# Kernel tuning notes

Measured on AMD Instinct MI355X. Metric: run time of the kernel, lower is better.

## Reference

```python
import jax, jax.numpy as jnp
import numpy as np

B, S, K = 4, 2048, 8
N_NEURONS, N_BASIS, RANK = 64, 32, 8
D_MODEL, D_HID = 256, 1024


def setup_inputs() -> dict:
    key = jax.random.key(0)
    ks = jax.random.split(key, 10)
    x = jax.random.normal(ks[0], (B, S, D_MODEL), dtype=jnp.float32)
    neuron_idx = jax.random.randint(ks[1], (B, S, K), 0, N_NEURONS)
    w = jax.random.uniform(ks[2], (B, S, K), dtype=jnp.float32)
    neuron_weights = w / jnp.sum(w, axis=-1, keepdims=True)  # softmax-like routing weights
    neuron_recipes = jax.random.normal(ks[3], (N_NEURONS, N_BASIS), dtype=jnp.float32) * 0.5
    sc = 0.1
    basis_A1 = jax.random.normal(ks[4], (N_BASIS, 16, RANK, 8), dtype=jnp.float32) * sc
    basis_A2 = jax.random.normal(ks[5], (N_BASIS, RANK, 16, 8), dtype=jnp.float32) * sc
    basis_B1 = jax.random.normal(ks[6], (N_BASIS, 8, RANK, 32), dtype=jnp.float32) * sc
    basis_B2 = jax.random.normal(ks[7], (N_BASIS, RANK, 8, 32), dtype=jnp.float32) * sc
    w_down_w = jax.random.normal(ks[8], (D_HID, D_MODEL), dtype=jnp.float32) * (1.0 / np.sqrt(D_HID))
    w_down_b = jnp.zeros((D_MODEL,), dtype=jnp.float32)
    return {
        "x": x, "neuron_idx": neuron_idx, "neuron_weights": neuron_weights,
        "neuron_recipes": neuron_recipes,
        "basis_A1": basis_A1, "basis_A2": basis_A2,
        "basis_B1": basis_B1, "basis_B2": basis_B2,
        "w_down_w": w_down_w, "w_down_b": w_down_b,
    }


def reference(x, neuron_idx, neuron_weights, neuron_recipes,
              basis_A1, basis_A2, basis_B1, basis_B2, w_down_w, w_down_b):
    Bt, St, D = x.shape
    # --- routing: gather recipes of selected neurons, softmax, weighted-combine ---
    sel = neuron_recipes[neuron_idx]                       # [B,S,k,n_basis]
    sel = jax.nn.softmax(sel, axis=-1)
    wr = jnp.einsum('bskn,bsk->bsn', sel, neuron_weights)  # [B,S,n_basis]
    # --- build per-token TT cores from basis banks (get_neuron_tt_cores) ---
    cA1 = jnp.einsum('bsn,nirk->bsirk', wr, basis_A1)      # [B,S,16,r,8]
    cA2 = jnp.einsum('bsn,nrjl->bsrjl', wr, basis_A2)      # [B,S,r,16,8]
    cB1 = jnp.einsum('bsn,nirk->bsirk', wr, basis_B1)      # [B,S,8,r,32]
    cB2 = jnp.einsum('bsn,nrjl->bsrjl', wr, basis_B2)      # [B,S,r,8,32]
    # --- TT FFN: 256 -> 64 ---
    x_fold = x.reshape(Bt, St, 16, 16)
    temp = jnp.einsum('bsij,bsirk->bsjrk', x_fold, cA1)
    h = jnp.einsum('bsjrk,bsrjl->bskl', temp, cA2).reshape(Bt, St, 64)
    # --- TT FFN: 64 -> 1024 ---
    h_fold = h.reshape(Bt, St, 8, 8)
    temp = jnp.einsum('bsij,bsirk->bsjrk', h_fold, cB1)
    out = jnp.einsum('bsjrk,bsrjl->bskl', temp, cB2).reshape(Bt, St, D_HID)
    out = jax.nn.gelu(out, approximate=False)              # torch F.gelu default = exact erf
    return out @ w_down_w + w_down_b                       # [B,S,256]
```

## Files before the change

kernel.cpp:

```cpp
#include <hip/hip_runtime.h>
#include <math.h>


typedef unsigned short u16;
typedef __attribute__((ext_vector_type(8))) __bf16 bf16x8;
typedef __attribute__((ext_vector_type(4))) float f32x4;
union ABCast { float4 f; bf16x8 v; };
union BFBits { __bf16 b; u16 u; };
union Pack8 { u16 u[8]; float4 f; };

__device__ __forceinline__ float gelu_exact(float v) {
    return 0.5f * v * (1.0f + erff(v * 0.70710678118654752440f));
}
__device__ __forceinline__ u16 f2bf_bits(float f) { BFBits c; c.b = (__bf16)f; return c.u; }
__device__ __forceinline__ float bfbits2f(u16 u) { BFBits c; c.u = u; return (float)c.b; }

__global__ __launch_bounds__(64) void k_route(
    const int* __restrict__ nidx, const float* __restrict__ nw,
    const float* __restrict__ recipes, float* __restrict__ wr_out,
    u16* __restrict__ wrAh, u16* __restrict__ wrAl)
{
    const int t = blockIdx.x * 64 + threadIdx.x;
    float acc[32];
#pragma unroll
    for (int n = 0; n < 32; n++) acc[n] = 0.f;
#pragma unroll
    for (int k = 0; k < 8; k++) {
        const int   id = nidx[t * 8 + k];
        const float wk = nw[t * 8 + k];
        const float4* row = (const float4*)(recipes + id * 32);
        float v[32];
#pragma unroll
        for (int q = 0; q < 8; q++) {
            float4 f = row[q];
            v[q*4+0] = f.x; v[q*4+1] = f.y; v[q*4+2] = f.z; v[q*4+3] = f.w;
        }
        float m = v[0];
#pragma unroll
        for (int n = 1; n < 32; n++) m = fmaxf(m, v[n]);
        float s = 0.f;
#pragma unroll
        for (int n = 0; n < 32; n++) { float e = expf(v[n] - m); v[n] = e; s += e; }
        const float iv = wk / s;
#pragma unroll
        for (int n = 0; n < 32; n++) acc[n] += v[n] * iv;
    }
    float4* o = (float4*)(wr_out + t * 32);
#pragma unroll
    for (int q = 0; q < 8; q++)
        o[q] = make_float4(acc[q*4+0], acc[q*4+1], acc[q*4+2], acc[q*4+3]);

    const int tg16 = t >> 4, tl = t & 15;
#pragma unroll
    for (int c = 0; c < 4; c++) {
        Pack8 ph, pl;
#pragma unroll
        for (int e = 0; e < 8; e++) {
            const float v = acc[c*8 + e];
            const u16 hb = f2bf_bits(v);
            ph.u[e] = hb;
            pl.u[e] = f2bf_bits(v - bfbits2f(hb));
        }
        const int lane = c * 16 + tl;
        *(float4*)(wrAh + (tg16*64 + lane)*8) = ph.f;
        *(float4*)(wrAl + (tg16*64 + lane)*8) = pl.f;
    }
}

__global__ __launch_bounds__(512) void k_stageA(
    const float* __restrict__ x, const float* __restrict__ wr,
    const float* __restrict__ A1, const float* __restrict__ A2,
    float* __restrict__ h_out)
{
    __shared__ float ca[8 * 1024];
    __shared__ float tl[8 * 1088];
    const int tid = threadIdx.x;
    const int t0  = blockIdx.x * 8;
    {
        const int e2 = tid * 2;
        float2 c[8];
#pragma unroll
        for (int tt = 0; tt < 8; tt++) c[tt] = make_float2(0.f, 0.f);
#pragma unroll 4
        for (int n = 0; n < 32; n++) {
            const float2 a = *(const float2*)(A1 + n * 1024 + e2);
#pragma unroll
            for (int tt = 0; tt < 8; tt++) {
                const float s = wr[(t0 + tt) * 32 + n];
                c[tt].x += s * a.x; c[tt].y += s * a.y;
            }
        }
#pragma unroll
        for (int tt = 0; tt < 8; tt++) *(float2*)(ca + tt * 1024 + e2) = c[tt];
    }
    __syncthreads();
    {
        const int t = tid >> 6, g = tid & 63, j = g >> 2, eh = g & 3;
        float xr[16];
#pragma unroll
        for (int i = 0; i < 16; i++) xr[i] = x[(t0 + t) * 256 + i * 16 + j];
        float tr[16];
#pragma unroll
        for (int q = 0; q < 16; q++) tr[q] = 0.f;
#pragma unroll
        for (int i = 0; i < 16; i++) {
            const float xv = xr[i];
#pragma unroll
            for (int q = 0; q < 4; q++) {
                const float4 cv = *(const float4*)(ca + t * 1024 + i * 64 + eh * 16 + q * 4);
                tr[q*4+0] += xv * cv.x; tr[q*4+1] += xv * cv.y;
                tr[q*4+2] += xv * cv.z; tr[q*4+3] += xv * cv.w;
            }
        }
#pragma unroll
        for (int q = 0; q < 4; q++)
            *(float4*)(tl + t * 1088 + j * 68 + eh * 16 + q * 4) =
                make_float4(tr[q*4+0], tr[q*4+1], tr[q*4+2], tr[q*4+3]);
    }
    __syncthreads();
    {
        const int e2 = tid * 2;
        float2 c[8];
#pragma unroll
        for (int tt = 0; tt < 8; tt++) c[tt] = make_float2(0.f, 0.f);
#pragma unroll 4
        for (int n = 0; n < 32; n++) {
            const float2 a = *(const float2*)(A2 + n * 1024 + e2);
#pragma unroll
            for (int tt = 0; tt < 8; tt++) {
                const float s = wr[(t0 + tt) * 32 + n];
                c[tt].x += s * a.x; c[tt].y += s * a.y;
            }
        }
#pragma unroll
        for (int tt = 0; tt < 8; tt++) *(float2*)(ca + tt * 1024 + e2) = c[tt];
    }
    __syncthreads();
    {
        const int t = tid >> 6, g = tid & 63, k = g >> 3, l = g & 7;
        float acc = 0.f;
#pragma unroll
        for (int j = 0; j < 16; j++) {
#pragma unroll
            for (int r = 0; r < 8; r++) {
                acc += tl[t * 1088 + j * 68 + r * 8 + k] *
                       ca[t * 1024 + r * 128 + j * 8 + l];
            }
        }
        h_out[(t0 + t) * 64 + g] = acc;
    }
}

__global__ __launch_bounds__(256) void k_bsplit(
    const float* __restrict__ B1, const float* __restrict__ B2,
    u16* __restrict__ o1h, u16* __restrict__ o1l,
    u16* __restrict__ o2h, u16* __restrict__ o2l)
{
    const int slot = blockIdx.x * 256 + threadIdx.x;
    const int bank = slot >> 13, r = (slot >> 10) & 7, g = (slot >> 6) & 15, l = slot & 63;
    const int c = l & 15, nb = 8 * (l >> 4);
    const int base = (bank == 0)
        ? ((g >> 1) * 256 + r * 32 + (g & 1) * 16 + c)
        : (r * 256 + (g >> 1) * 32 + (g & 1) * 16 + c);
    const float* S = (bank ? B2 : B1) + base + nb * 2048;
    Pack8 ph, pl;
#pragma unroll
    for (int e = 0; e < 8; e++) {
        const float v = S[e * 2048];
        const u16 hb = f2bf_bits(v);
        ph.u[e] = hb;
        pl.u[e] = f2bf_bits(v - bfbits2f(hb));
    }
    const int d = ((r * 16 + g) * 64 + l) * 8;
    *(float4*)((bank ? o2h : o1h) + d) = ph.f;
    *(float4*)((bank ? o2l : o1l) + d) = pl.f;
}

__global__ __launch_bounds__(256) void k_wsplit(
    const float* __restrict__ W, u16* __restrict__ wfh, u16* __restrict__ wfl)
{
    const int slot = blockIdx.x * 256 + threadIdx.x;
    const int ng = slot >> 11, kc = (slot >> 6) & 31, l = slot & 63;
    const float* S = W + (kc * 32 + 8 * (l >> 4)) * 256 + ng * 16 + (l & 15);
    Pack8 ph, pl;
#pragma unroll
    for (int e = 0; e < 8; e++) {
        const float v = S[e * 256];
        const u16 hb = f2bf_bits(v);
        ph.u[e] = hb;
        pl.u[e] = f2bf_bits(v - bfbits2f(hb));
    }
    const int d = ((ng * 32 + kc) * 64 + l) * 8;
    *(float4*)(wfh + d) = ph.f;
    *(float4*)(wfl + d) = pl.f;
}

__global__ __launch_bounds__(1024, 2) void k_fusedB(
    const float* __restrict__ hin,
    const u16* __restrict__ wrAh, const u16* __restrict__ wrAl,
    const u16* __restrict__ bf1h, const u16* __restrict__ bf1l,
    const u16* __restrict__ bf2h, const u16* __restrict__ bf2l,
    const u16* __restrict__ wfh, const u16* __restrict__ wfl,
    const float* __restrict__ bias, float* __restrict__ y)
{
    __shared__ __align__(16) unsigned char smem[81920];
    float* cb1 = (float*)smem;
    float* cb2 = cb1 + 2 * 16 * 256;
    float* t2  = cb2 + 2 * 16 * 256;
    u16* gAh = (u16*)smem;
    u16* gAl = gAh + 16384;

    const int tid = threadIdx.x;
    const int l   = tid & 63;
    const int w   = tid >> 6;
    const int tg  = blockIdx.x;
    const int t0  = tg * 16;

    const int j2 = l >> 3, k42 = l & 7;
    const int k0 = (l & 7) * 4, l0 = (l >> 3) * 4;

    float hreg[8];
#pragma unroll
    for (int i = 0; i < 8; i++) hreg[i] = hin[(t0 + w) * 64 + i * 8 + j2];

    ABCast cu;
    cu.f = *(const float4*)(wrAh + (tg * 64 + l) * 8); const bf16x8 wra_h = cu.v;
    cu.f = *(const float4*)(wrAl + (tg * 64 + l) * 8); const bf16x8 wra_l = cu.v;

    const bool isB2 = (w >= 8);
    const u16* bsrc_h = isB2 ? bf2h : bf1h;
    const u16* bsrc_l = isB2 ? bf2l : bf1l;
    float* cdst0 = isB2 ? cb2 : cb1;
    const int g0 = (w & 7) * 2;

    float o[4][4];
#pragma unroll
    for (int a = 0; a < 4; a++)
#pragma unroll
        for (int li = 0; li < 4; li++) o[a][li] = 0.f;

    float4 pbh0, pbl0, pbh1, pbl1;
#define LOADB(R) {                                                              \
    const int rb_ = (R) * 16;                                                   \
    pbh0 = *(const float4*)(bsrc_h + ((rb_ + g0 + 0)*64 + l)*8);                \
    pbl0 = *(const float4*)(bsrc_l + ((rb_ + g0 + 0)*64 + l)*8);                \
    pbh1 = *(const float4*)(bsrc_h + ((rb_ + g0 + 1)*64 + l)*8);                \
    pbl1 = *(const float4*)(bsrc_l + ((rb_ + g0 + 1)*64 + l)*8); }
#define BUILD(BSEL) {                                                           \
    float* cdst = cdst0 + (BSEL) * 4096;                                        \
    __builtin_amdgcn_s_setprio(1);                                              \
    ABCast ch_, cl_;                                                            \
    ch_.f = pbh0; cl_.f = pbl0;                                                 \
    f32x4 cc = {0.f, 0.f, 0.f, 0.f};                                            \
    cc = __builtin_amdgcn_mfma_f32_16x16x32_bf16(wra_h, ch_.v, cc, 0, 0, 0);    \
    cc = __builtin_amdgcn_mfma_f32_16x16x32_bf16(wra_h, cl_.v, cc, 0, 0, 0);    \
    cc = __builtin_amdgcn_mfma_f32_16x16x32_bf16(wra_l, ch_.v, cc, 0, 0, 0);    \
    ch_.f = pbh1; cl_.f = pbl1;                                                 \
    f32x4 cc2 = {0.f, 0.f, 0.f, 0.f};                                           \
    cc2 = __builtin_amdgcn_mfma_f32_16x16x32_bf16(wra_h, ch_.v, cc2, 0, 0, 0);  \
    cc2 = __builtin_amdgcn_mfma_f32_16x16x32_bf16(wra_h, cl_.v, cc2, 0, 0, 0);  \
    cc2 = __builtin_amdgcn_mfma_f32_16x16x32_bf16(wra_l, ch_.v, cc2, 0, 0, 0);  \
    __builtin_amdgcn_s_setprio(0);                                              \
    { const int gg = g0;                                                        \
      float* cd = cdst + (gg >> 1) * 32 + (gg & 1) * 16 + (l & 15);             \
      _Pragma("unroll")                                                         \
      for (int reg = 0; reg < 4; reg++) cd[(4 * (l >> 4) + reg) * 256] = cc[reg]; } \
    { const int gg = g0 + 1;                                                    \
      float* cd = cdst + (gg >> 1) * 32 + (gg & 1) * 16 + (l & 15);             \
      _Pragma("unroll")                                                         \
      for (int reg = 0; reg < 4; reg++) cd[(4 * (l >> 4) + reg) * 256] = cc2[reg]; } }

    LOADB(0);
    BUILD(0);
    LOADB(1);
    __syncthreads();

#pragma unroll 1
    for (int r = 0; r < 8; r++) {
        if (r < 7) {
            BUILD((r + 1) & 1);
            if (r < 6) LOADB(r + 2);
        }

        {
            const float* c1b = cb1 + (r & 1) * 4096 + w * 256;
            float4 acc = make_float4(0.f, 0.f, 0.f, 0.f);
#pragma unroll
            for (int i = 0; i < 8; i++) {
                const float  hv = hreg[i];
                const float4 cv = *(const float4*)(c1b + i * 32 + k42 * 4);
                acc.x += hv * cv.x; acc.y += hv * cv.y;
                acc.z += hv * cv.z; acc.w += hv * cv.w;
            }
            *(float4*)(t2 + w * 256 + j2 * 32 + k42 * 4) = acc;
        }

        {
            const float* c2b = cb2 + (r & 1) * 4096 + w * 256;
#pragma unroll
            for (int j = 0; j < 8; j++) {
                const float4 tv4 = *(const float4*)(t2 + w * 256 + j * 32 + k0);
                const float4 cv4 = *(const float4*)(c2b + j * 32 + l0);
                const float tv[4] = {tv4.x, tv4.y, tv4.z, tv4.w};
                const float cv[4] = {cv4.x, cv4.y, cv4.z, cv4.w};
#pragma unroll
                for (int a = 0; a < 4; a++)
#pragma unroll
                    for (int li = 0; li < 4; li++)
                        o[a][li] += tv[a] * cv[li];
            }
        }
        __syncthreads();
    }
#undef LOADB
#undef BUILD

    {
        const int lane2 = (l0 >> 3) * 16 + w;
        const int e0 = l0 & 7;
#pragma unroll
        for (int a = 0; a < 4; a++) {
            u16 hv[4], lv[4];
#pragma unroll
            for (int li = 0; li < 4; li++) {
                const float v = gelu_exact(o[a][li]);
                const u16 hb = f2bf_bits(v);
                hv[li] = hb;
                lv[li] = f2bf_bits(v - bfbits2f(hb));
            }
            const int step = k0 + a;
            *(ushort4*)(gAh + (step * 64 + lane2) * 8 + e0) = make_ushort4(hv[0], hv[1], hv[2], hv[3]);
            *(ushort4*)(gAl + (step * 64 + lane2) * 8 + e0) = make_ushort4(lv[0], lv[1], lv[2], lv[3]);
        }
    }
    __syncthreads();

    if (w < 8) {
        f32x4 dacc0 = {0.f, 0.f, 0.f, 0.f}, dacc1 = {0.f, 0.f, 0.f, 0.f};
        const int wb0 = w * 16384 + l * 8;
        const int wb1 = (w + 8) * 16384 + l * 8;
#pragma unroll 2
        for (int kc = 0; kc < 32; kc++) {
            cu.f = *(const float4*)(gAh + (kc * 64 + l) * 8); const bf16x8 ah = cu.v;
            cu.f = *(const float4*)(gAl + (kc * 64 + l) * 8); const bf16x8 al = cu.v;
            ABCast c0, c1, c2, c3;
            c0.f = *(const float4*)(wfh + wb0 + kc * 512); const bf16x8 bh0 = c0.v;
            c1.f = *(const float4*)(wfl + wb0 + kc * 512); const bf16x8 bl0 = c1.v;
            c2.f = *(const float4*)(wfh + wb1 + kc * 512); const bf16x8 bh1 = c2.v;
            c3.f = *(const float4*)(wfl + wb1 + kc * 512); const bf16x8 bl1 = c3.v;
            dacc0 = __builtin_amdgcn_mfma_f32_16x16x32_bf16(ah, bh0, dacc0, 0, 0, 0);
            dacc0 = __builtin_amdgcn_mfma_f32_16x16x32_bf16(ah, bl0, dacc0, 0, 0, 0);
            dacc0 = __builtin_amdgcn_mfma_f32_16x16x32_bf16(al, bh0, dacc0, 0, 0, 0);
            dacc1 = __builtin_amdgcn_mfma_f32_16x16x32_bf16(ah, bh1, dacc1, 0, 0, 0);
            dacc1 = __builtin_amdgcn_mfma_f32_16x16x32_bf16(ah, bl1, dacc1, 0, 0, 0);
            dacc1 = __builtin_amdgcn_mfma_f32_16x16x32_bf16(al, bh1, dacc1, 0, 0, 0);
        }
        const int n0 = w * 16 + (l & 15);
        const int n1 = (w + 8) * 16 + (l & 15);
        const float b0 = bias[n0], b1 = bias[n1];
        const int tb = t0 + 4 * (l >> 4);
#pragma unroll
        for (int reg = 0; reg < 4; reg++) {
            y[(tb + reg) * 256 + n0] = dacc0[reg] + b0;
            y[(tb + reg) * 256 + n1] = dacc1[reg] + b1;
        }
    }
}

extern "C" void kernel_launch(void* const* d_in, const int* in_sizes, int n_in,
                              void* d_out, int out_size, void* d_ws, size_t ws_size,
                              hipStream_t stream)
{
    const float* x    = (const float*)d_in[0];
    const int*   nidx = (const int*)  d_in[1];
    const float* nw   = (const float*)d_in[2];
    const float* rec  = (const float*)d_in[3];
    const float* A1   = (const float*)d_in[4];
    const float* A2   = (const float*)d_in[5];
    const float* B1   = (const float*)d_in[6];
    const float* B2   = (const float*)d_in[7];
    const float* Wd   = (const float*)d_in[8];
    const float* bd   = (const float*)d_in[9];
    float* y  = (float*)d_out;

    float* wr  = (float*)d_ws;
    float* h   = wr + 8192 * 32;
    u16* wrAh  = (u16*)(h + 8192 * 64);
    u16* wrAl  = wrAh + 262144;
    u16* b1h   = wrAl + 262144;
    u16* b1l   = b1h + 65536;
    u16* b2h   = b1l + 65536;
    u16* b2l   = b2h + 65536;
    u16* wfh   = b2l + 65536;
    u16* wfl   = wfh + 262144;

    k_route <<<128,  64,   0, stream>>>(nidx, nw, rec, wr, wrAh, wrAl);
    k_stageA<<<1024, 512,  0, stream>>>(x, wr, A1, A2, h);
    k_bsplit<<<64,   256,  0, stream>>>(B1, B2, b1h, b1l, b2h, b2l);
    k_wsplit<<<128,  256,  0, stream>>>(Wd, wfh, wfl);
    k_fusedB<<<512,  1024, 0, stream>>>(h, wrAh, wrAl, b1h, b1l, b2h, b2l, wfh, wfl, bd, y);
}
```

Baseline: 99.09 us.

## Move second TT contraction in fusedB onto 32x32 bf16 MFMA with split precision

Replaces the scalar FP32 outer-product accumulation of the cB2 contraction with 32x32x16 bf16 MFMAs on hi/lo split operands. The temp and cB2 core tiles are stored to LDS as bf16 pairs in a padded layout, and two ranks are batched per MFMA window. This targets the VALU cost of the 8x4x4 FMA loop per rank. In exchange it raises LDS use from 80KB to about 128KB, which may cut occupancy below two blocks per CU, and it adds conversion work and slight precision loss.

```diff
diff --git a/kernel.cpp b/kernel.cpp
--- a/kernel.cpp
+++ b/kernel.cpp
@@ -5,6 +5,7 @@
 typedef unsigned short u16;
 typedef __attribute__((ext_vector_type(8))) __bf16 bf16x8;
 typedef __attribute__((ext_vector_type(4))) float f32x4;
+typedef __attribute__((ext_vector_type(16))) float f32x16;
 union ABCast { float4 f; bf16x8 v; };
 union BFBits { __bf16 b; u16 u; };
 union Pack8 { u16 u[8]; float4 f; };
@@ -203,10 +204,10 @@
     const u16* __restrict__ wfh, const u16* __restrict__ wfl,
     const float* __restrict__ bias, float* __restrict__ y)
 {
-    __shared__ __align__(16) unsigned char smem[81920];
+    __shared__ __align__(16) unsigned char smem[131584];
     float* cb1 = (float*)smem;
-    float* cb2 = cb1 + 2 * 16 * 256;
-    float* t2  = cb2 + 2 * 16 * 256;
+    u16* t2p = (u16*)(smem + 32768);
+    u16* c2p = (u16*)(smem + 82176);
     u16* gAh = (u16*)smem;
     u16* gAl = gAh + 16384;
 
@@ -215,13 +216,15 @@
     const int w   = tid >> 6;
     const int tg  = blockIdx.x;
     const int t0  = tg * 16;
-
-    const int j2 = l >> 3, k42 = l & 7;
-    const int k0 = (l & 7) * 4, l0 = (l >> 3) * 4;
-
-    float hreg[8];
-#pragma unroll
-    for (int i = 0; i < 8; i++) hreg[i] = hin[(t0 + w) * 64 + i * 8 + j2];
+    const int jh  = l >> 5;
+    const int kP  = l & 31;
+
+    float hreg[32];
+#pragma unroll
+    for (int i = 0; i < 8; i++)
+#pragma unroll
+        for (int jj = 0; jj < 4; jj++)
+            hreg[i*4+jj] = hin[(t0 + w) * 64 + i * 8 + jh * 4 + jj];
 
     ABCast cu;
     cu.f = *(const float4*)(wrAh + (tg * 64 + l) * 8); const bf16x8 wra_h = cu.v;
@@ -230,14 +233,10 @@
     const bool isB2 = (w >= 8);
     const u16* bsrc_h = isB2 ? bf2h : bf1h;
     const u16* bsrc_l = isB2 ? bf2l : bf1l;
-    float* cdst0 = isB2 ? cb2 : cb1;
     const int g0 = (w & 7) * 2;
 
-    float o[4][4];
-#pragma unroll
-    for (int a = 0; a < 4; a++)
-#pragma unroll
-        for (int li = 0; li < 4; li++) o[a][li] = 0.f;
+    f32x16 accw = {0.f,0.f,0.f,0.f,0.f,0.f,0.f,0.f,0.f,0.f,0.f,0.f,0.f,0.f,0.f,0.f};
+    f32x4 ccA, ccB;
 
     float4 pbh0, pbl0, pbh1, pbl1;
 #define LOADB(R) {                                                              \
@@ -247,28 +246,54 @@
     pbh1 = *(const float4*)(bsrc_h + ((rb_ + g0 + 1)*64 + l)*8);                \
     pbl1 = *(const float4*)(bsrc_l + ((rb_ + g0 + 1)*64 + l)*8); }
 #define BUILD(BSEL) {                                                           \
-    float* cdst = cdst0 + (BSEL) * 4096;                                        \
+    ABCast ch_, cl_;                                                            \
     __builtin_amdgcn_s_setprio(1);                                              \
-    ABCast ch_, cl_;                                                            \
     ch_.f = pbh0; cl_.f = pbl0;                                                 \
-    f32x4 cc = {0.f, 0.f, 0.f, 0.f};                                            \
-    cc = __builtin_amdgcn_mfma_f32_16x16x32_bf16(wra_h, ch_.v, cc, 0, 0, 0);    \
-    cc = __builtin_amdgcn_mfma_f32_16x16x32_bf16(wra_h, cl_.v, cc, 0, 0, 0);    \
-    cc = __builtin_amdgcn_mfma_f32_16x16x32_bf16(wra_l, ch_.v, cc, 0, 0, 0);    \
+    f32x4 t0_ = {0.f, 0.f, 0.f, 0.f};                                           \
+    t0_ = __builtin_amdgcn_mfma_f32_16x16x32_bf16(wra_h, ch_.v, t0_, 0, 0, 0);  \
+    t0_ = __builtin_amdgcn_mfma_f32_16x16x32_bf16(wra_h, cl_.v, t0_, 0, 0, 0);  \
+    t0_ = __builtin_amdgcn_mfma_f32_16x16x32_bf16(wra_l, ch_.v, t0_, 0, 0, 0);  \
     ch_.f = pbh1; cl_.f = pbl1;                                                 \
-    f32x4 cc2 = {0.f, 0.f, 0.f, 0.f};                                           \
-    cc2 = __builtin_amdgcn_mfma_f32_16x16x32_bf16(wra_h, ch_.v, cc2, 0, 0, 0);  \
-    cc2 = __builtin_amdgcn_mfma_f32_16x16x32_bf16(wra_h, cl_.v, cc2, 0, 0, 0);  \
-    cc2 = __builtin_amdgcn_mfma_f32_16x16x32_bf16(wra_l, ch_.v, cc2, 0, 0, 0);  \
+    f32x4 t1_ = {0.f, 0.f, 0.f, 0.f};                                           \
+    t1_ = __builtin_amdgcn_mfma_f32_16x16x32_bf16(wra_h, ch_.v, t1_, 0, 0, 0);  \
+    t1_ = __builtin_amdgcn_mfma_f32_16x16x32_bf16(wra_h, cl_.v, t1_, 0, 0, 0);  \
+    t1_ = __builtin_amdgcn_mfma_f32_16x16x32_bf16(wra_l, ch_.v, t1_, 0, 0, 0);  \
     __builtin_amdgcn_s_setprio(0);                                              \
-    { const int gg = g0;                                                        \
-      float* cd = cdst + (gg >> 1) * 32 + (gg & 1) * 16 + (l & 15);             \
-      _Pragma("unroll")                                                         \
-      for (int reg = 0; reg < 4; reg++) cd[(4 * (l >> 4) + reg) * 256] = cc[reg]; } \
-    { const int gg = g0 + 1;                                                    \
-      float* cd = cdst + (gg >> 1) * 32 + (gg & 1) * 16 + (l & 15);             \
-      _Pragma("unroll")                                                         \
-      for (int reg = 0; reg < 4; reg++) cd[(4 * (l >> 4) + reg) * 256] = cc2[reg]; } }
+    ccA = t0_; ccB = t1_;                                                       \
+    if (w < 8) {                                                                \
+        float* cdst = cb1 + (BSEL) * 4096;                                      \
+        { const int gg = g0;                                                    \
+          float* cd = cdst + (gg >> 1) * 32 + (gg & 1) * 16 + (l & 15);         \
+          _Pragma("unroll")                                                     \
+          for (int rg = 0; rg < 4; rg++) cd[(4*(l>>4)+rg)*256] = ccA[rg]; }     \
+        { const int gg = g0 + 1;                                                \
+          float* cd = cdst + (gg >> 1) * 32 + (gg & 1) * 16 + (l & 15);         \
+          _Pragma("unroll")                                                     \
+          for (int rg = 0; rg < 4; rg++) cd[(4*(l>>4)+rg)*256] = ccB[rg]; } } }
+#define STORECB2(R) if (w >= 8) {                                               \
+    _Pragma("unroll")                                                           \
+    for (int gi = 0; gi < 2; gi++) {                                            \
+        const int gg = g0 + gi, jj_ = gg >> 1;                                  \
+        const int lc_ = (gg & 1) * 16 + (l & 15);                               \
+        _Pragma("unroll")                                                       \
+        for (int rg = 0; rg < 4; rg++) {                                        \
+            const float vv = gi ? ccB[rg] : ccA[rg];                            \
+            const u16 hb = f2bf_bits(vv);                                       \
+            const u16 lb = f2bf_bits(vv - bfbits2f(hb));                        \
+            const int tok = 4 * (l >> 4) + rg;                                  \
+            const int idx = tok * 1544 + lc_ * 24 + 8 * ((R) & 1) + jj_;        \
+            c2p[idx] = hb; c2p[idx + 768] = lb;                                 \
+        } } }
+#define WINDOW() {                                                              \
+    ABCast ua, ub;                                                              \
+    const int ab = w * 1544 + kP * 24 + 8 * jh;                                 \
+    ua.f = *(const float4*)(t2p + ab);       const bf16x8 Ah = ua.v;            \
+    ua.f = *(const float4*)(t2p + ab + 768); const bf16x8 Al = ua.v;            \
+    ub.f = *(const float4*)(c2p + ab);       const bf16x8 Bh = ub.v;            \
+    ub.f = *(const float4*)(c2p + ab + 768); const bf16x8 Bl = ub.v;            \
+    accw = __builtin_amdgcn_mfma_f32_32x32x16_bf16(Ah, Bh, accw, 0, 0, 0);      \
+    accw = __builtin_amdgcn_mfma_f32_32x32x16_bf16(Ah, Bl, accw, 0, 0, 0);      \
+    accw = __builtin_amdgcn_mfma_f32_32x32x16_bf16(Al, Bh, accw, 0, 0, 0); }
 
     LOADB(0);
     BUILD(0);
@@ -277,60 +302,46 @@
 
 #pragma unroll 1
     for (int r = 0; r < 8; r++) {
+        if (r > 0 && (r & 1) == 0) {
+            WINDOW();
+            __syncthreads();
+        }
+        STORECB2(r);
         if (r < 7) {
             BUILD((r + 1) & 1);
             if (r < 6) LOADB(r + 2);
         }
-
         {
             const float* c1b = cb1 + (r & 1) * 4096 + w * 256;
-            float4 acc = make_float4(0.f, 0.f, 0.f, 0.f);
+            float tv0 = 0.f, tv1 = 0.f, tv2 = 0.f, tv3 = 0.f;
 #pragma unroll
             for (int i = 0; i < 8; i++) {
-                const float  hv = hreg[i];
-                const float4 cv = *(const float4*)(c1b + i * 32 + k42 * 4);
-                acc.x += hv * cv.x; acc.y += hv * cv.y;
-                acc.z += hv * cv.z; acc.w += hv * cv.w;
+                const float cv = c1b[i * 32 + kP];
+                tv0 += hreg[i*4+0] * cv; tv1 += hreg[i*4+1] * cv;
+                tv2 += hreg[i*4+2] * cv; tv3 += hreg[i*4+3] * cv;
             }
-            *(float4*)(t2 + w * 256 + j2 * 32 + k42 * 4) = acc;
-        }
-
-        {
-            const float* c2b = cb2 + (r & 1) * 4096 + w * 256;
-#pragma unroll
-            for (int j = 0; j < 8; j++) {
-                const float4 tv4 = *(const float4*)(t2 + w * 256 + j * 32 + k0);
-                const float4 cv4 = *(const float4*)(c2b + j * 32 + l0);
-                const float tv[4] = {tv4.x, tv4.y, tv4.z, tv4.w};
-                const float cv[4] = {cv4.x, cv4.y, cv4.z, cv4.w};
-#pragma unroll
-                for (int a = 0; a < 4; a++)
-#pragma unroll
-                    for (int li = 0; li < 4; li++)
-                        o[a][li] += tv[a] * cv[li];
-            }
+            const u16 h0 = f2bf_bits(tv0), h1 = f2bf_bits(tv1),
+                      h2 = f2bf_bits(tv2), h3 = f2bf_bits(tv3);
+            const u16 q0 = f2bf_bits(tv0 - bfbits2f(h0)), q1 = f2bf_bits(tv1 - bfbits2f(h1)),
+                      q2 = f2bf_bits(tv2 - bfbits2f(h2)), q3 = f2bf_bits(tv3 - bfbits2f(h3));
+            const int tb = w * 1544 + kP * 24 + 8 * (r & 1) + jh * 4;
+            *(ushort4*)(t2p + tb)       = make_ushort4(h0, h1, h2, h3);
+            *(ushort4*)(t2p + tb + 768) = make_ushort4(q0, q1, q2, q3);
         }
         __syncthreads();
     }
-#undef LOADB
-#undef BUILD
+    WINDOW();
+    __syncthreads();
 
     {
-        const int lane2 = (l0 >> 3) * 16 + w;
-        const int e0 = l0 & 7;
-#pragma unroll
-        for (int a = 0; a < 4; a++) {
-            u16 hv[4], lv[4];
-#pragma unroll
-            for (int li = 0; li < 4; li++) {
-                const float v = gelu_exact(o[a][li]);
-                const u16 hb = f2bf_bits(v);
-                hv[li] = hb;
-                lv[li] = f2bf_bits(v - bfbits2f(hb));
-            }
-            const int step = k0 + a;
-            *(ushort4*)(gAh + (step * 64 + lane2) * 8 + e0) = make_ushort4(hv[0], hv[1], hv[2], hv[3]);
-            *(ushort4*)(gAl + (step * 64 + lane2) * 8 + e0) = make_ushort4(lv[0], lv[1], lv[2], lv[3]);
+#pragma unroll
+        for (int rg = 0; rg < 16; rg++) {
+            const int kk = (rg & 3) + 8 * (rg >> 2) + 4 * jh;
+            const float v = gelu_exact(accw[rg]);
+            const u16 hb = f2bf_bits(v);
+            const u16 lb = f2bf_bits(v - bfbits2f(hb));
+            const int idx = (kk * 64 + (kP >> 3) * 16 + w) * 8 + (kP & 7);
+            gAh[idx] = hb; gAl[idx] = lb;
         }
     }
     __syncthreads();
@@ -360,11 +371,15 @@
         const float b0 = bias[n0], b1 = bias[n1];
         const int tb = t0 + 4 * (l >> 4);
 #pragma unroll
-        for (int reg = 0; reg < 4; reg++) {
-            y[(tb + reg) * 256 + n0] = dacc0[reg] + b0;
-            y[(tb + reg) * 256 + n1] = dacc1[reg] + b1;
-        }
-    }
+        for (int rg = 0; rg < 4; rg++) {
+            y[(tb + rg) * 256 + n0] = dacc0[rg] + b0;
+            y[(tb + rg) * 256 + n1] = dacc1[rg] + b1;
+        }
+    }
+#undef LOADB
+#undef BUILD
+#undef STORECB2
+#undef WINDOW
 }
 
 extern "C" void kernel_launch(void* const* d_in, const int* in_sizes, int n_in,
```

Result: no change. 98.06 us (-1.0%).
